# Kernel tuning notes

Measured on AMD Instinct MI355X. Metric: run time of the kernel, lower is better.

Reference implementation:

```python
import jax, jax.numpy as jnp
import numpy as np

N_NODES = 100000


def gcn_conv(x, edge_index, W, b):
    """PyG GCNConv: add self-loops, symmetric deg^{-1/2} A deg^{-1/2} aggregation.

    x: [N, Fin], edge_index: [2, E] int (row 0 = src, row 1 = dst).
    Transform first (Fin -> Fout), then gather-normalize-scatter at Fout.
    """
    n = x.shape[0]
    loops = jnp.arange(n, dtype=edge_index.dtype)
    src = jnp.concatenate([edge_index[0], loops])
    dst = jnp.concatenate([edge_index[1], loops])
    # in-degree with self-loops (all edge weights = 1)
    deg = jax.ops.segment_sum(jnp.ones_like(dst, dtype=x.dtype), dst, num_segments=n)
    dinv = jax.lax.rsqrt(deg)  # deg >= 1 thanks to self-loops
    norm = dinv[src] * dinv[dst]  # [E+N]
    h = x @ W  # [N, Fout] dense transform before sparse aggregation
    msgs = norm[:, None] * h[src]  # gather + normalize
    out = jax.ops.segment_sum(msgs, dst, num_segments=n)  # scatter-add
    return out + b


def setup_inputs() -> dict:
    key = jax.random.key(0)
    ks = jax.random.split(key, 8)
    N, E, Fin, H, C = N_NODES, 1600000, 256, 64, 11
    x = jax.random.normal(ks[0], (N, Fin), dtype=jnp.float32)
    edge_index = jax.random.randint(ks[1], (2, E), 0, N, dtype=jnp.int64)
    s1 = 1.0 / np.sqrt(Fin)
    s2 = 1.0 / np.sqrt(H)
    W1 = jax.random.uniform(ks[2], (Fin, H), jnp.float32, -s1, s1)
    b1 = jnp.zeros((H,), jnp.float32)
    W2 = jax.random.uniform(ks[3], (H, H), jnp.float32, -s2, s2)
    b2 = jnp.zeros((H,), jnp.float32)
    Wfc = jax.random.uniform(ks[4], (H, C), jnp.float32, -s2, s2)
    bfc = jax.random.uniform(ks[5], (C,), jnp.float32, -s2, s2)
    return {"x": x, "edge_index": edge_index, "W1": W1, "b1": b1,
            "W2": W2, "b2": b2, "Wfc": Wfc, "bfc": bfc}


def reference(x, edge_index, W1, b1, W2, b2, Wfc, bfc):
    h = jax.nn.relu(gcn_conv(x, edge_index, W1, b1))
    h = jax.nn.relu(gcn_conv(h, edge_index, W2, b2))
    return h @ Wfc + bfc  # [N, 11]
```

## Files before the change

kernel.cpp:

```cpp
#include <hip/hip_runtime.h>
#include <hip/hip_fp16.h>

#define NFEAT 64
#define SCAN_CHUNK 2048

typedef _Float16 half8 __attribute__((ext_vector_type(8)));
typedef float f32x4 __attribute__((ext_vector_type(4)));

__device__ __forceinline__ void gll16(const float* g, float* l) {
    __builtin_amdgcn_global_load_lds(
        (const __attribute__((address_space(1))) unsigned int*)g,
        (__attribute__((address_space(3))) unsigned int*)l, 16, 0, 0);
}

__device__ __forceinline__ __half2 bch(unsigned int u) {
    return __builtin_bit_cast(__half2, u);
}

__global__ void k_cvtW(const float* __restrict__ W, __half* __restrict__ Wt, int K) {
    int idx = blockIdx.x * 256 + threadIdx.x;
    if (idx >= 64 * K) return;
    int n = idx / K;
    int k = idx % K;
    Wt[idx] = __float2half(W[(size_t)k * NFEAT + n]);
}

template<int K, bool SCALE, bool CNT>
__global__ __launch_bounds__(256) void k_gemm_x(
    const float* __restrict__ A, const __half* __restrict__ Wt,
    const float* __restrict__ dinv, __half* __restrict__ H, int M,
    const int* __restrict__ eiDst, int* __restrict__ counts,
    int* __restrict__ rank, int E)
{
    int tid = threadIdx.x;
    int gemmIdx;
    if (CNT) {
        int bid = blockIdx.x;
        if (bid & 1) {
            int t = (((bid >> 1) * 256) + tid) * 4;
            if (t + 3 < E) {
                int4 d = *(const int4*)(eiDst + t);
                int r0 = atomicAdd(&counts[d.x], 1);
                int r1 = atomicAdd(&counts[d.y], 1);
                int r2 = atomicAdd(&counts[d.z], 1);
                int r3 = atomicAdd(&counts[d.w], 1);
                *(int4*)(rank + t) = make_int4(r0, r1, r2, r3);
            } else {
                for (int e = t; e < E; ++e)
                    rank[e] = atomicAdd(&counts[eiDst[e]], 1);
            }
            return;
        }
        gemmIdx = bid >> 1;
    } else {
        gemmIdx = blockIdx.x;
    }

    const int BM = 64, BK = 32;
    __shared__ float As[2 * BM * BK];

    int w = tid >> 6, lane = tid & 63;
    int q = lane >> 4, n16 = lane & 15;
    int m0 = gemmIdx * BM;

    auto stage = [&](int k0, int buf) {
#pragma unroll
        for (int rep = 0; rep < 2; ++rep) {
            int cb = (w * 2 + rep) * 64;
            int s = cb + lane;
            int m = s >> 3;
            int kk = (s & 7) ^ (m & 7);
            int row = m0 + m; if (row > M - 1) row = M - 1;
            gll16(A + (size_t)row * K + k0 + kk * 4,
                  &As[buf * (BM * BK) + cb * 4]);
        }
    };

    stage(0, 0);

    f32x4 acc[4];
#pragma unroll
    for (int nt = 0; nt < 4; ++nt) acc[nt] = (f32x4)(0.f);

    const __half* wp = Wt + (size_t)n16 * K + q * 8;

    const int T = K / BK;
    for (int kt = 0; kt < T; ++kt) {
        __syncthreads();
        if (kt + 1 < T) stage((kt + 1) * BK, (kt + 1) & 1);
        const float* As_ = &As[(kt & 1) * (BM * BK)];

        int ml = w * 16 + n16;
        int e0 = (2 * q) ^ (ml & 7);
        int e1 = (2 * q + 1) ^ (ml & 7);
        float4 f0 = *(const float4*)&As_[(ml * 8 + e0) * 4];
        float4 f1 = *(const float4*)&As_[(ml * 8 + e1) * 4];
        float fv[8] = {f0.x, f0.y, f0.z, f0.w, f1.x, f1.y, f1.z, f1.w};
        half8 ahi, alo;
#pragma unroll
        for (int j = 0; j < 8; ++j) {
            _Float16 hi = (_Float16)fv[j];
            ahi[j] = hi;
            alo[j] = (_Float16)(fv[j] - (float)hi);
        }
#pragma unroll
        for (int nt = 0; nt < 4; ++nt) {
            uint4 u = *(const uint4*)(wp + (size_t)(nt * 16) * K + kt * BK);
            half8 b = __builtin_bit_cast(half8, u);
            acc[nt] = __builtin_amdgcn_mfma_f32_16x16x32_f16(ahi, b, acc[nt], 0, 0, 0);
            acc[nt] = __builtin_amdgcn_mfma_f32_16x16x32_f16(alo, b, acc[nt], 0, 0, 0);
        }
        __syncthreads();
    }

#pragma unroll
    for (int reg = 0; reg < 4; ++reg) {
        int row = m0 + w * 16 + q * 4 + reg;
        if (row < M) {
            float di = SCALE ? dinv[row] : 1.0f;
#pragma unroll
            for (int nt = 0; nt < 4; ++nt)
                H[(size_t)row * NFEAT + nt * 16 + n16] =
                    __float2half(di * acc[nt][reg]);
        }
    }
}

__global__ __launch_bounds__(256) void k_dinv_scan(
    const int* __restrict__ counts, int* __restrict__ bsums,
    float* __restrict__ dinv, int n, int nbScan)
{
    __shared__ int red[256];
    int bid = blockIdx.x;
    int tid = threadIdx.x;
    if (bid < nbScan) {
        int base = bid * SCAN_CHUNK + tid * 8;
        int s = 0;
#pragma unroll
        for (int i = 0; i < 8; ++i) {
            int idx = base + i;
            s += (idx < n) ? counts[idx] : 0;
        }
        red[tid] = s;
        __syncthreads();
        for (int off = 128; off; off >>= 1) {
            if (tid < off) red[tid] += red[tid + off];
            __syncthreads();
        }
        if (tid == 0) bsums[bid] = red[0];
    } else {
        int i = (bid - nbScan) * 256 + tid;
        if (i < n) dinv[i] = rsqrtf((float)(counts[i] + 1));
    }
}

__global__ void k_scan_sums(int* bsums, int nb) {
    __shared__ int ts[64];
    int tid = threadIdx.x;
    if (tid < 64) ts[tid] = (tid < nb) ? bsums[tid] : 0;
    __syncthreads();
    if (tid == 0) {
        int run = 0;
        for (int i = 0; i < nb; ++i) { int t = ts[i]; ts[i] = run; run += t; }
    }
    __syncthreads();
    if (tid < nb) bsums[tid] = ts[tid];
}

__global__ __launch_bounds__(256) void k_scan_final(const int* __restrict__ counts,
                                                    const int* __restrict__ bsums,
                                                    int* __restrict__ rowptr, int n) {
    __shared__ int ts[256];
    int tid = threadIdx.x;
    int base0 = blockIdx.x * SCAN_CHUNK + tid * 8;
    int v[8], c[8];
    int s = 0;
#pragma unroll
    for (int i = 0; i < 8; ++i) {
        int idx = base0 + i;
        c[i] = (idx < n) ? counts[idx] : 0;
        v[i] = s;
        s += c[i];
    }
    ts[tid] = s;
    __syncthreads();
    for (int off = 1; off < 256; off <<= 1) {
        int t = (tid >= off) ? ts[tid - off] : 0;
        __syncthreads();
        if (tid >= off) ts[tid] += t;
        __syncthreads();
    }
    int texcl = ts[tid] - s;
    int base = bsums[blockIdx.x] + texcl;
#pragma unroll
    for (int i = 0; i < 8; ++i) {
        int idx = base0 + i;
        if (idx < n) {
            int val = base + v[i];
            rowptr[idx] = val;
            if (idx == n - 1) rowptr[n] = val + c[i];
        }
    }
}

__global__ __launch_bounds__(256) void k_build_scale(
    const int* __restrict__ ei, const int* __restrict__ rank,
    const int* __restrict__ rowptr, int* __restrict__ col, int E,
    __half* __restrict__ A, const float* __restrict__ dinv, int N, int gE)
{
    int bid = blockIdx.x;
    if (bid < gE) {
        int e = bid * 256 + threadIdx.x;
        if (e >= E) return;
        int src = ei[e];
        int dst = ei[(size_t)E + e];
        col[rowptr[dst] + rank[e]] = src;
    } else {
        int i = (bid - gE) * 256 + threadIdx.x;
        if (i >= N * 8) return;
        float di = dinv[i >> 3];
        uint4* p = (uint4*)A + i;
        uint4 u = *p;
        auto sc = [&](unsigned int x) {
            float2 f = __half22float2(bch(x));
            return __builtin_bit_cast(unsigned int,
                   __float22half2_rn(make_float2(f.x * di, f.y * di)));
        };
        u.x = sc(u.x); u.y = sc(u.y); u.z = sc(u.z); u.w = sc(u.w);
        *p = u;
    }
}

template<bool FC>
__global__ __launch_bounds__(256) void k_aggr(
    const __half* __restrict__ h, const int* __restrict__ rowptr,
    const int* __restrict__ col, const float* __restrict__ dinv,
    const float* __restrict__ bias, const float* __restrict__ Wfc,
    const float* __restrict__ bfc, float* __restrict__ out, int n)
{
    __shared__ float Wl[NFEAT * 11 + 11];
    int tid = threadIdx.x;
    if (FC) {
        for (int i = tid; i < NFEAT * 11; i += 256) Wl[i] = Wfc[i];
        if (tid < 11) Wl[NFEAT * 11 + tid] = bfc[tid];
        __syncthreads();
    }
    int lane = tid & 63;
    int li = lane & 7;
    int fi = li << 3;
    int r = blockIdx.x * 32 + ((tid >> 6) << 3) + (lane >> 3);
    bool valid = r < n;

    int beg = 0, end = 0;
    if (valid) { beg = rowptr[r]; end = rowptr[r + 1]; }

    const __half* hp = h + fi;
    auto ld = [&](int src) { return *(const uint4*)(hp + (size_t)src * NFEAT); };

    float a0 = 0.f, a1 = 0.f, a2 = 0.f, a3 = 0.f,
          a4 = 0.f, a5 = 0.f, a6 = 0.f, a7 = 0.f;
    auto addu = [&](uint4 u) {
        float2 f0 = __half22float2(bch(u.x));
        float2 f1 = __half22float2(bch(u.y));
        float2 f2 = __half22float2(bch(u.z));
        float2 f3 = __half22float2(bch(u.w));
        a0 += f0.x; a1 += f0.y; a2 += f1.x; a3 += f1.y;
        a4 += f2.x; a5 += f2.y; a6 += f3.x; a7 += f3.y;
    };

    if (valid) addu(ld(r));
    int j = beg;
    for (; j + 1 < end; j += 2) {
        uint4 u0 = ld(col[j]);
        uint4 u1 = ld(col[j + 1]);
        uint4 s;
        s.x = __builtin_bit_cast(unsigned int, __hadd2(bch(u0.x), bch(u1.x)));
        s.y = __builtin_bit_cast(unsigned int, __hadd2(bch(u0.y), bch(u1.y)));
        s.z = __builtin_bit_cast(unsigned int, __hadd2(bch(u0.z), bch(u1.z)));
        s.w = __builtin_bit_cast(unsigned int, __hadd2(bch(u0.w), bch(u1.w)));
        addu(s);
    }
    if (j < end) addu(ld(col[j]));

    if (!valid) return;
    float di = dinv[r];
    float t0 = fmaxf(bias[fi + 0] + di * a0, 0.f);
    float t1 = fmaxf(bias[fi + 1] + di * a1, 0.f);
    float t2 = fmaxf(bias[fi + 2] + di * a2, 0.f);
    float t3 = fmaxf(bias[fi + 3] + di * a3, 0.f);
    float t4 = fmaxf(bias[fi + 4] + di * a4, 0.f);
    float t5 = fmaxf(bias[fi + 5] + di * a5, 0.f);
    float t6 = fmaxf(bias[fi + 6] + di * a6, 0.f);
    float t7 = fmaxf(bias[fi + 7] + di * a7, 0.f);

    if (!FC) {
        float4 lo = make_float4(t0, t1, t2, t3);
        float4 hi = make_float4(t4, t5, t6, t7);
        float* op = out + (size_t)r * NFEAT + fi;
        *(float4*)op = lo;
        *(float4*)(op + 4) = hi;
    } else {
#pragma unroll
        for (int c = 0; c < 11; ++c) {
            const float* wc = &Wl[fi * 11 + c];
            float p = t0 * wc[0] + t1 * wc[11] + t2 * wc[22] + t3 * wc[33]
                    + t4 * wc[44] + t5 * wc[55] + t6 * wc[66] + t7 * wc[77];
            p += __shfl_xor(p, 1, 64);
            p += __shfl_xor(p, 2, 64);
            p += __shfl_xor(p, 4, 64);
            if (li == 0) out[(size_t)r * 11 + c] = p + Wl[NFEAT * 11 + c];
        }
    }
}

extern "C" void kernel_launch(void* const* d_in, const int* in_sizes, int n_in,
                              void* d_out, int out_size, void* d_ws, size_t ws_size,
                              hipStream_t stream) {
    const float* x   = (const float*)d_in[0];
    const int*   ei  = (const int*)d_in[1];
    const float* W1  = (const float*)d_in[2];
    const float* b1  = (const float*)d_in[3];
    const float* W2  = (const float*)d_in[4];
    const float* b2  = (const float*)d_in[5];
    const float* Wfc = (const float*)d_in[6];
    const float* bfc = (const float*)d_in[7];
    float* out = (float*)d_out;

    const int Fin = 256;
    int N = in_sizes[0] / Fin;
    int E = in_sizes[1] / 2;

    char* ws = (char*)d_ws;
    size_t off = 0;
    auto alloc = [&](size_t bytes) { void* p = ws + off; off = (off + bytes + 255) & ~(size_t)255; return p; };
    int*    counts = (int*)   alloc((size_t)N * 4);
    int*    rowptr = (int*)   alloc((size_t)(N + 1) * 4);
    float*  dinv   = (float*) alloc((size_t)N * 4);
    int*    bsums  = (int*)   alloc(64 * 4);
    int*    rank   = (int*)   alloc((size_t)E * 4);
    int*    col    = (int*)   alloc((size_t)E * 4);
    __half* Wt1    = (__half*)alloc((size_t)64 * 256 * 2);
    __half* Wt2    = (__half*)alloc((size_t)64 * 64 * 2);
    __half* A      = (__half*)alloc((size_t)N * NFEAT * 2);
    float*  B      = (float*) alloc((size_t)N * NFEAT * 4);

    int gE = (E + 255) / 256;
    int gb = (N + 63) / 64;
    int gA = (N + 31) / 32;
    int gS = (N * 8 + 255) / 256;
    int nb = (N + SCAN_CHUNK - 1) / SCAN_CHUNK;
    int gN = (N + 255) / 256;

    hipMemsetAsync(counts, 0, (size_t)N * 4, stream);
    k_cvtW<<<(64 * 256 + 255) / 256, 256, 0, stream>>>(W1, Wt1, 256);
    k_cvtW<<<(64 * 64 + 255) / 256, 256, 0, stream>>>(W2, Wt2, 64);

    k_gemm_x<256, false, true><<<gb * 2, 256, 0, stream>>>(
        x, Wt1, nullptr, A, N, ei + E, counts, rank, E);

    k_dinv_scan<<<nb + gN, 256, 0, stream>>>(counts, bsums, dinv, N, nb);
    k_scan_sums<<<1, 64, 0, stream>>>(bsums, nb);
    k_scan_final<<<nb, 256, 0, stream>>>(counts, bsums, rowptr, N);

    k_build_scale<<<gE + gS, 256, 0, stream>>>(ei, rank, rowptr, col, E, A, dinv, N, gE);

    k_aggr<false><<<gA, 256, 0, stream>>>(A, rowptr, col, dinv, b1, nullptr, nullptr, B, N);

    k_gemm_x<64, true, false><<<gb, 256, 0, stream>>>(
        B, Wt2, dinv, A, N, nullptr, nullptr, nullptr, 0);
    k_aggr<true><<<gA, 256, 0, stream>>>(A, rowptr, col, dinv, b2, Wfc, bfc, out, N);
}
```

Measured before the change: 356.5 us.

## Privatize degree-count atomics per XCD and merge the partial counts in the scan

Edge in-degree counting now writes to 8 per-XCD copies of the counter array. Each copy is selected by the hardware XCC_ID register and updated with workgroup-scope relaxed atomics, so the atomics can resolve in the local L2 instead of at device scope. The rank is packed as (local rank << 3 | xcd). The scan kernel merges the 8 partial counts, writes per-node per-XCD base offsets, and computes dinv. The CSR build uses those offsets to place each edge. This adds a larger memset plus extra base8 read/write traffic (reusing buffer B as scratch), and it relies on workgroup-scope atomics staying coherent across CUs within one XCD.

After: 379.4 us. 6.4% more time.

```diff
diff --git a/kernel.cpp b/kernel.cpp
--- a/kernel.cpp
+++ b/kernel.cpp
@@ -37,17 +37,25 @@
     if (CNT) {
         int bid = blockIdx.x;
         if (bid & 1) {
+            unsigned xcd;
+            asm("s_getreg_b32 %0, hwreg(HW_REG_XCC_ID)" : "=s"(xcd));
+            xcd &= 7;
+            int* cb = counts + (size_t)xcd * M;
+            auto at = [&](int d) {
+                return (__hip_atomic_fetch_add(&cb[d], 1, __ATOMIC_RELAXED,
+                        __HIP_MEMORY_SCOPE_WORKGROUP) << 3) | (int)xcd;
+            };
             int t = (((bid >> 1) * 256) + tid) * 4;
             if (t + 3 < E) {
                 int4 d = *(const int4*)(eiDst + t);
-                int r0 = atomicAdd(&counts[d.x], 1);
-                int r1 = atomicAdd(&counts[d.y], 1);
-                int r2 = atomicAdd(&counts[d.z], 1);
-                int r3 = atomicAdd(&counts[d.w], 1);
+                int r0 = at(d.x);
+                int r1 = at(d.y);
+                int r2 = at(d.z);
+                int r3 = at(d.w);
                 *(int4*)(rank + t) = make_int4(r0, r1, r2, r3);
             } else {
                 for (int e = t; e < E; ++e)
-                    rank[e] = atomicAdd(&counts[eiDst[e]], 1);
+                    rank[e] = at(eiDst[e]);
             }
             return;
         }
@@ -127,31 +135,71 @@
 }
 
 __global__ __launch_bounds__(256) void k_dinv_scan(
-    const int* __restrict__ counts, int* __restrict__ bsums,
-    float* __restrict__ dinv, int n, int nbScan)
+    const int* __restrict__ counts8, int* __restrict__ counts,
+    int* __restrict__ base8, int* __restrict__ bsums,
+    float* __restrict__ dinv, int n)
 {
     __shared__ int red[256];
+    int tid = threadIdx.x;
     int bid = blockIdx.x;
-    int tid = threadIdx.x;
-    if (bid < nbScan) {
-        int base = bid * SCAN_CHUNK + tid * 8;
-        int s = 0;
+    int base0 = bid * SCAN_CHUNK + tid * 8;
+    int ssum = 0;
+
+    if (base0 + 7 < n) {
+        int tot[8];
+        int bv[8][8];
+#pragma unroll
+        for (int i = 0; i < 8; ++i) tot[i] = 0;
+#pragma unroll
+        for (int s = 0; s < 8; ++s) {
+            const int4* p = (const int4*)(counts8 + (size_t)s * n + base0);
+            int4 c0 = p[0], c1 = p[1];
+            int c[8] = {c0.x, c0.y, c0.z, c0.w, c1.x, c1.y, c1.z, c1.w};
+#pragma unroll
+            for (int i = 0; i < 8; ++i) { bv[i][s] = tot[i]; tot[i] += c[i]; }
+        }
 #pragma unroll
         for (int i = 0; i < 8; ++i) {
-            int idx = base + i;
-            s += (idx < n) ? counts[idx] : 0;
-        }
-        red[tid] = s;
-        __syncthreads();
-        for (int off = 128; off; off >>= 1) {
-            if (tid < off) red[tid] += red[tid + off];
-            __syncthreads();
-        }
-        if (tid == 0) bsums[bid] = red[0];
+            *(int4*)(base8 + (size_t)(base0 + i) * 8) =
+                make_int4(bv[i][0], bv[i][1], bv[i][2], bv[i][3]);
+            *(int4*)(base8 + (size_t)(base0 + i) * 8 + 4) =
+                make_int4(bv[i][4], bv[i][5], bv[i][6], bv[i][7]);
+        }
+        *(int4*)(counts + base0)     = make_int4(tot[0], tot[1], tot[2], tot[3]);
+        *(int4*)(counts + base0 + 4) = make_int4(tot[4], tot[5], tot[6], tot[7]);
+        *(float4*)(dinv + base0) = make_float4(
+            rsqrtf((float)(tot[0] + 1)), rsqrtf((float)(tot[1] + 1)),
+            rsqrtf((float)(tot[2] + 1)), rsqrtf((float)(tot[3] + 1)));
+        *(float4*)(dinv + base0 + 4) = make_float4(
+            rsqrtf((float)(tot[4] + 1)), rsqrtf((float)(tot[5] + 1)),
+            rsqrtf((float)(tot[6] + 1)), rsqrtf((float)(tot[7] + 1)));
+#pragma unroll
+        for (int i = 0; i < 8; ++i) ssum += tot[i];
     } else {
-        int i = (bid - nbScan) * 256 + tid;
-        if (i < n) dinv[i] = rsqrtf((float)(counts[i] + 1));
-    }
+#pragma unroll
+        for (int i = 0; i < 8; ++i) {
+            int idx = base0 + i;
+            if (idx < n) {
+                int t = 0;
+#pragma unroll
+                for (int s = 0; s < 8; ++s) {
+                    base8[(size_t)idx * 8 + s] = t;
+                    t += counts8[(size_t)s * n + idx];
+                }
+                counts[idx] = t;
+                dinv[idx] = rsqrtf((float)(t + 1));
+                ssum += t;
+            }
+        }
+    }
+
+    red[tid] = ssum;
+    __syncthreads();
+    for (int off = 128; off; off >>= 1) {
+        if (tid < off) red[tid] += red[tid + off];
+        __syncthreads();
+    }
+    if (tid == 0) bsums[bid] = red[0];
 }
 
 __global__ void k_scan_sums(int* bsums, int nb) {
@@ -205,7 +253,8 @@
 
 __global__ __launch_bounds__(256) void k_build_scale(
     const int* __restrict__ ei, const int* __restrict__ rank,
-    const int* __restrict__ rowptr, int* __restrict__ col, int E,
+    const int* __restrict__ rowptr, const int* __restrict__ base8,
+    int* __restrict__ col, int E,
     __half* __restrict__ A, const float* __restrict__ dinv, int N, int gE)
 {
     int bid = blockIdx.x;
@@ -214,7 +263,8 @@
         if (e >= E) return;
         int src = ei[e];
         int dst = ei[(size_t)E + e];
-        col[rowptr[dst] + rank[e]] = src;
+        int r = rank[e];
+        col[rowptr[dst] + base8[(size_t)dst * 8 + (r & 7)] + (r >> 3)] = src;
     } else {
         int i = (bid - gE) * 256 + threadIdx.x;
         if (i >= N * 8) return;
@@ -344,25 +394,27 @@
     __half* A      = (__half*)alloc((size_t)N * NFEAT * 2);
     float*  B      = (float*) alloc((size_t)N * NFEAT * 4);
 
+    int* counts8 = (int*)B;
+    int* base8   = (int*)B + (size_t)8 * N;
+
     int gE = (E + 255) / 256;
     int gb = (N + 63) / 64;
     int gA = (N + 31) / 32;
     int gS = (N * 8 + 255) / 256;
     int nb = (N + SCAN_CHUNK - 1) / SCAN_CHUNK;
-    int gN = (N + 255) / 256;
-
-    hipMemsetAsync(counts, 0, (size_t)N * 4, stream);
+
+    hipMemsetAsync(counts8, 0, (size_t)8 * N * 4, stream);
     k_cvtW<<<(64 * 256 + 255) / 256, 256, 0, stream>>>(W1, Wt1, 256);
     k_cvtW<<<(64 * 64 + 255) / 256, 256, 0, stream>>>(W2, Wt2, 64);
 
     k_gemm_x<256, false, true><<<gb * 2, 256, 0, stream>>>(
-        x, Wt1, nullptr, A, N, ei + E, counts, rank, E);
-
-    k_dinv_scan<<<nb + gN, 256, 0, stream>>>(counts, bsums, dinv, N, nb);
+        x, Wt1, nullptr, A, N, ei + E, counts8, rank, E);
+
+    k_dinv_scan<<<nb, 256, 0, stream>>>(counts8, counts, base8, bsums, dinv, N);
     k_scan_sums<<<1, 64, 0, stream>>>(bsums, nb);
     k_scan_final<<<nb, 256, 0, stream>>>(counts, bsums, rowptr, N);
 
-    k_build_scale<<<gE + gS, 256, 0, stream>>>(ei, rank, rowptr, col, E, A, dinv, N, gE);
+    k_build_scale<<<gE + gS, 256, 0, stream>>>(ei, rank, rowptr, base8, col, E, A, dinv, N, gE);
 
     k_aggr<false><<<gA, 256, 0, stream>>>(A, rowptr, col, dinv, b1, nullptr, nullptr, B, N);
 
```

## Build CSR via two-level bucket sort with LDS histograms instead of global atomics

Applied to the files above, without the earlier changes.

Replaces the global per-node atomic counting and rank-based CSR fill with a two-pass bucket sort. Edges are histogrammed per chunk into 256-node buckets in shared memory, scanned, and scattered into bucket order. Each bucket is then sorted locally in shared memory to produce rowptr, dinv, col and the dinv scaling of the first transform. This removes contended global atomics, the memset and several scan launches, and keeps the random accesses within cache-sized buckets. The cost is an extra pass over an intermediate edge array stored in the B buffer, and reliance on EBUF-sized shared staging with a global fallback.

Result: faster. 327.1 us (-8.2%).

```diff
diff --git a/kernel.cpp b/kernel.cpp
--- a/kernel.cpp
+++ b/kernel.cpp
@@ -2,7 +2,8 @@
 #include <hip/hip_fp16.h>
 
 #define NFEAT 64
-#define SCAN_CHUNK 2048
+#define CE 8192
+#define EBUF 4608
 
 typedef _Float16 half8 __attribute__((ext_vector_type(8)));
 typedef float f32x4 __attribute__((ext_vector_type(4)));
@@ -29,35 +30,36 @@
 __global__ __launch_bounds__(256) void k_gemm_x(
     const float* __restrict__ A, const __half* __restrict__ Wt,
     const float* __restrict__ dinv, __half* __restrict__ H, int M,
-    const int* __restrict__ eiDst, int* __restrict__ counts,
-    int* __restrict__ rank, int E)
+    const int* __restrict__ eiDst, int* __restrict__ hist, int E)
 {
+    const int BM = 64, BK = 32;
+    __shared__ float As[2 * BM * BK];
+
     int tid = threadIdx.x;
     int gemmIdx;
     if (CNT) {
         int bid = blockIdx.x;
-        if (bid & 1) {
-            int t = (((bid >> 1) * 256) + tid) * 4;
-            if (t + 3 < E) {
-                int4 d = *(const int4*)(eiDst + t);
-                int r0 = atomicAdd(&counts[d.x], 1);
-                int r1 = atomicAdd(&counts[d.y], 1);
-                int r2 = atomicAdd(&counts[d.z], 1);
-                int r3 = atomicAdd(&counts[d.w], 1);
-                *(int4*)(rank + t) = make_int4(r0, r1, r2, r3);
-            } else {
-                for (int e = t; e < E; ++e)
-                    rank[e] = atomicAdd(&counts[eiDst[e]], 1);
-            }
+        int nbkt = (M + 255) >> 8;
+        if (bid % 9 == 8) {
+            int c = bid / 9;
+            int base = c * CE;
+            if (base >= E) return;
+            int* hb = (int*)As;
+            for (int i = tid; i < nbkt; i += 256) hb[i] = 0;
+            __syncthreads();
+            int hi = min(base + CE, E);
+            for (int e = base + tid; e < hi; e += 256)
+                atomicAdd(&hb[eiDst[e] >> 8], 1);
+            __syncthreads();
+            for (int i = tid; i < nbkt; i += 256)
+                hist[(size_t)c * nbkt + i] = hb[i];
             return;
         }
-        gemmIdx = bid >> 1;
+        gemmIdx = bid - bid / 9;
     } else {
         gemmIdx = blockIdx.x;
     }
-
-    const int BM = 64, BK = 32;
-    __shared__ float As[2 * BM * BK];
+    if (gemmIdx * BM >= M) return;
 
     int w = tid >> 6, lane = tid & 63;
     int q = lane >> 4, n16 = lane & 15;
@@ -126,108 +128,130 @@
     }
 }
 
-__global__ __launch_bounds__(256) void k_dinv_scan(
-    const int* __restrict__ counts, int* __restrict__ bsums,
-    float* __restrict__ dinv, int n, int nbScan)
+__global__ __launch_bounds__(256) void k_scanB(int* __restrict__ hist,
+                                               int* __restrict__ cntB,
+                                               int nchk, int nbkt) {
+    __shared__ int hb[256];
+    int b = blockIdx.x, tid = threadIdx.x;
+    int v = (tid < nchk) ? hist[(size_t)tid * nbkt + b] : 0;
+    hb[tid] = v;
+    __syncthreads();
+    for (int off = 1; off < 256; off <<= 1) {
+        int t = (tid >= off) ? hb[tid - off] : 0;
+        __syncthreads();
+        if (tid >= off) hb[tid] += t;
+        __syncthreads();
+    }
+    if (tid < nchk) hist[(size_t)tid * nbkt + b] = hb[tid] - v;
+    if (tid == 255) cntB[b] = hb[255];
+}
+
+__global__ __launch_bounds__(256) void k_scanC(const int* __restrict__ cntB,
+                                               int* __restrict__ bb, int nbkt) {
+    __shared__ int hb[256];
+    int tid = threadIdx.x;
+    int i0 = 2 * tid, i1 = 2 * tid + 1;
+    int a0 = (i0 < nbkt) ? cntB[i0] : 0;
+    int a1 = (i1 < nbkt) ? cntB[i1] : 0;
+    hb[tid] = a0 + a1;
+    __syncthreads();
+    for (int off = 1; off < 256; off <<= 1) {
+        int t = (tid >= off) ? hb[tid - off] : 0;
+        __syncthreads();
+        if (tid >= off) hb[tid] += t;
+        __syncthreads();
+    }
+    int excl = hb[tid] - (a0 + a1);
+    if (i0 <= nbkt) bb[i0] = excl;
+    if (i1 <= nbkt) bb[i1] = excl + a0;
+}
+
+__global__ __launch_bounds__(256) void k_scatter(
+    const int* __restrict__ ei, const int* __restrict__ hist,
+    const int* __restrict__ bb, int2* __restrict__ E2, int E, int nbkt)
 {
-    __shared__ int red[256];
-    int bid = blockIdx.x;
-    int tid = threadIdx.x;
-    if (bid < nbScan) {
-        int base = bid * SCAN_CHUNK + tid * 8;
-        int s = 0;
-#pragma unroll
-        for (int i = 0; i < 8; ++i) {
-            int idx = base + i;
-            s += (idx < n) ? counts[idx] : 0;
-        }
-        red[tid] = s;
-        __syncthreads();
-        for (int off = 128; off; off >>= 1) {
-            if (tid < off) red[tid] += red[tid + off];
-            __syncthreads();
-        }
-        if (tid == 0) bsums[bid] = red[0];
-    } else {
-        int i = (bid - nbScan) * 256 + tid;
-        if (i < n) dinv[i] = rsqrtf((float)(counts[i] + 1));
-    }
-}
-
-__global__ void k_scan_sums(int* bsums, int nb) {
-    __shared__ int ts[64];
-    int tid = threadIdx.x;
-    if (tid < 64) ts[tid] = (tid < nb) ? bsums[tid] : 0;
-    __syncthreads();
-    if (tid == 0) {
-        int run = 0;
-        for (int i = 0; i < nb; ++i) { int t = ts[i]; ts[i] = run; run += t; }
-    }
-    __syncthreads();
-    if (tid < nb) bsums[tid] = ts[tid];
-}
-
-__global__ __launch_bounds__(256) void k_scan_final(const int* __restrict__ counts,
-                                                    const int* __restrict__ bsums,
-                                                    int* __restrict__ rowptr, int n) {
-    __shared__ int ts[256];
-    int tid = threadIdx.x;
-    int base0 = blockIdx.x * SCAN_CHUNK + tid * 8;
-    int v[8], c[8];
-    int s = 0;
-#pragma unroll
-    for (int i = 0; i < 8; ++i) {
-        int idx = base0 + i;
-        c[i] = (idx < n) ? counts[idx] : 0;
-        v[i] = s;
-        s += c[i];
-    }
-    ts[tid] = s;
-    __syncthreads();
+    __shared__ int ptr[512];
+    int c = blockIdx.x, tid = threadIdx.x;
+    for (int i = tid; i < nbkt; i += 256)
+        ptr[i] = bb[i] + hist[(size_t)c * nbkt + i];
+    __syncthreads();
+    int base = c * CE, hi = min(base + CE, E);
+    for (int e = base + tid; e < hi; e += 256) {
+        int s = ei[e];
+        int d = ei[(size_t)E + e];
+        int p = atomicAdd(&ptr[d >> 8], 1);
+        E2[p] = make_int2(s, d);
+    }
+}
+
+__global__ __launch_bounds__(256) void k_csr(
+    const int2* __restrict__ E2, const int* __restrict__ bb,
+    int* __restrict__ rowptr, float* __restrict__ dinv, int* __restrict__ col,
+    __half* __restrict__ A, int N, int E)
+{
+    __shared__ int2 ebuf[EBUF];
+    __shared__ int cnt[256];
+    __shared__ float dl[256];
+    int b = blockIdx.x, tid = threadIdx.x;
+    int e0 = bb[b], e1 = bb[b + 1], ne = e1 - e0;
+    int nL = min(ne, EBUF);
+
+    cnt[tid] = 0;
+    __syncthreads();
+    for (int i = tid; i < nL; i += 256) {
+        int2 e = E2[e0 + i];
+        ebuf[i] = e;
+        atomicAdd(&cnt[e.y & 255], 1);
+    }
+    for (int i = nL + tid; i < ne; i += 256) {
+        int2 e = E2[e0 + i];
+        atomicAdd(&cnt[e.y & 255], 1);
+    }
+    __syncthreads();
+    int c = cnt[tid];
+    dl[tid] = rsqrtf((float)(c + 1));
     for (int off = 1; off < 256; off <<= 1) {
-        int t = (tid >= off) ? ts[tid - off] : 0;
-        __syncthreads();
-        if (tid >= off) ts[tid] += t;
-        __syncthreads();
-    }
-    int texcl = ts[tid] - s;
-    int base = bsums[blockIdx.x] + texcl;
-#pragma unroll
-    for (int i = 0; i < 8; ++i) {
-        int idx = base0 + i;
-        if (idx < n) {
-            int val = base + v[i];
-            rowptr[idx] = val;
-            if (idx == n - 1) rowptr[n] = val + c[i];
-        }
-    }
-}
-
-__global__ __launch_bounds__(256) void k_build_scale(
-    const int* __restrict__ ei, const int* __restrict__ rank,
-    const int* __restrict__ rowptr, int* __restrict__ col, int E,
-    __half* __restrict__ A, const float* __restrict__ dinv, int N, int gE)
-{
-    int bid = blockIdx.x;
-    if (bid < gE) {
-        int e = bid * 256 + threadIdx.x;
-        if (e >= E) return;
-        int src = ei[e];
-        int dst = ei[(size_t)E + e];
-        col[rowptr[dst] + rank[e]] = src;
-    } else {
-        int i = (bid - gE) * 256 + threadIdx.x;
-        if (i >= N * 8) return;
-        float di = dinv[i >> 3];
-        uint4* p = (uint4*)A + i;
-        uint4 u = *p;
-        auto sc = [&](unsigned int x) {
-            float2 f = __half22float2(bch(x));
-            return __builtin_bit_cast(unsigned int,
-                   __float22half2_rn(make_float2(f.x * di, f.y * di)));
-        };
-        u.x = sc(u.x); u.y = sc(u.y); u.z = sc(u.z); u.w = sc(u.w);
-        *p = u;
+        int t = (tid >= off) ? cnt[tid - off] : 0;
+        __syncthreads();
+        if (tid >= off) cnt[tid] += t;
+        __syncthreads();
+    }
+    int excl = cnt[tid] - c;
+    int node = b * 256 + tid;
+    if (node < N) {
+        rowptr[node] = e0 + excl;
+        dinv[node] = dl[tid];
+    }
+    if (b == 0 && tid == 0) rowptr[N] = E;
+    __syncthreads();
+    cnt[tid] = excl;
+    __syncthreads();
+    for (int i = tid; i < nL; i += 256) {
+        int2 e = ebuf[i];
+        int p = atomicAdd(&cnt[e.y & 255], 1);
+        col[e0 + p] = e.x;
+    }
+    for (int i = nL + tid; i < ne; i += 256) {
+        int2 e = E2[e0 + i];
+        int p = atomicAdd(&cnt[e.y & 255], 1);
+        col[e0 + p] = e.x;
+    }
+
+    for (int it = tid; it < 256 * 8; it += 256) {
+        int ln = it >> 3;
+        int node2 = b * 256 + ln;
+        if (node2 < N) {
+            float di = dl[ln];
+            uint4* p = (uint4*)A + (size_t)node2 * 8 + (it & 7);
+            uint4 u = *p;
+            auto sc = [&](unsigned int x) {
+                float2 f = __half22float2(bch(x));
+                return __builtin_bit_cast(unsigned int,
+                       __float22half2_rn(make_float2(f.x * di, f.y * di)));
+            };
+            u.x = sc(u.x); u.y = sc(u.y); u.z = sc(u.z); u.w = sc(u.w);
+            *p = u;
+        }
     }
 }
 
@@ -333,40 +357,41 @@
     char* ws = (char*)d_ws;
     size_t off = 0;
     auto alloc = [&](size_t bytes) { void* p = ws + off; off = (off + bytes + 255) & ~(size_t)255; return p; };
-    int*    counts = (int*)   alloc((size_t)N * 4);
     int*    rowptr = (int*)   alloc((size_t)(N + 1) * 4);
     float*  dinv   = (float*) alloc((size_t)N * 4);
-    int*    bsums  = (int*)   alloc(64 * 4);
-    int*    rank   = (int*)   alloc((size_t)E * 4);
     int*    col    = (int*)   alloc((size_t)E * 4);
     __half* Wt1    = (__half*)alloc((size_t)64 * 256 * 2);
     __half* Wt2    = (__half*)alloc((size_t)64 * 64 * 2);
     __half* A      = (__half*)alloc((size_t)N * NFEAT * 2);
     float*  B      = (float*) alloc((size_t)N * NFEAT * 4);
 
-    int gE = (E + 255) / 256;
-    int gb = (N + 63) / 64;
-    int gA = (N + 31) / 32;
-    int gS = (N * 8 + 255) / 256;
-    int nb = (N + SCAN_CHUNK - 1) / SCAN_CHUNK;
-    int gN = (N + 255) / 256;
-
-    hipMemsetAsync(counts, 0, (size_t)N * 4, stream);
+    int NBKT = (N + 255) >> 8;
+    int NCHK = (E + CE - 1) / CE;
+
+    int2* E2   = (int2*)B;
+    int*  hist = (int*)B + (size_t)2 * E;
+    int*  bb   = hist + (size_t)NCHK * NBKT;
+    int*  cntB = bb + NBKT + 1;
+
+    int gE2 = NCHK;
+    int gb  = (N + 63) / 64;
+    int gA  = (N + 31) / 32;
+    int g9  = 9 * max(NCHK, (gb + 7) / 8);
+
     k_cvtW<<<(64 * 256 + 255) / 256, 256, 0, stream>>>(W1, Wt1, 256);
     k_cvtW<<<(64 * 64 + 255) / 256, 256, 0, stream>>>(W2, Wt2, 64);
 
-    k_gemm_x<256, false, true><<<gb * 2, 256, 0, stream>>>(
-        x, Wt1, nullptr, A, N, ei + E, counts, rank, E);
-
-    k_dinv_scan<<<nb + gN, 256, 0, stream>>>(counts, bsums, dinv, N, nb);
-    k_scan_sums<<<1, 64, 0, stream>>>(bsums, nb);
-    k_scan_final<<<nb, 256, 0, stream>>>(counts, bsums, rowptr, N);
-
-    k_build_scale<<<gE + gS, 256, 0, stream>>>(ei, rank, rowptr, col, E, A, dinv, N, gE);
+    k_gemm_x<256, false, true><<<g9, 256, 0, stream>>>(
+        x, Wt1, nullptr, A, N, ei + E, hist, E);
+
+    k_scanB<<<NBKT, 256, 0, stream>>>(hist, cntB, NCHK, NBKT);
+    k_scanC<<<1, 256, 0, stream>>>(cntB, bb, NBKT);
+    k_scatter<<<gE2, 256, 0, stream>>>(ei, hist, bb, E2, E, NBKT);
+    k_csr<<<NBKT, 256, 0, stream>>>(E2, bb, rowptr, dinv, col, A, N, E);
 
     k_aggr<false><<<gA, 256, 0, stream>>>(A, rowptr, col, dinv, b1, nullptr, nullptr, B, N);
 
     k_gemm_x<64, true, false><<<gb, 256, 0, stream>>>(
-        B, Wt2, dinv, A, N, nullptr, nullptr, nullptr, 0);
+        B, Wt2, dinv, A, N, nullptr, nullptr, 0);
     k_aggr<true><<<gA, 256, 0, stream>>>(A, rowptr, col, dinv, b2, Wfc, bfc, out, N);
 }
```
